# Performance work log

Hardware: AMD Instinct MI355X
Metric: run time of the kernel (lower is better)

## Reference

```python
import jax, jax.numpy as jnp
import numpy as np

N = 50000        # nodes
E = 800000       # edges (avg degree 16)
F_IN = 128       # in_channels
HID = 32         # hidden_channels per head
H = 8            # heads
DH = HID * H     # 256, concat dim
NC = {'TL': 12, 'YL': 30, 'TS': 60, 'TZ': 120}
NEG_SLOPE = 0.2  # PyG GATConv default


def setup_inputs() -> dict:
    key = jax.random.key(0)
    ks = jax.random.split(key, 40)
    rn = lambda k, s, sc=0.1: jax.random.normal(k, s, jnp.float32) * sc
    inp = {}
    inp['x'] = jax.random.normal(ks[0], (N, F_IN), jnp.float32)
    inp['edge_index'] = jax.random.randint(ks[1], (2, E), 0, N, dtype=jnp.int64)
    # conv1: in -> H x HID (concat)
    inp['W1'] = rn(ks[2], (F_IN, DH)); inp['a1s'] = rn(ks[3], (H, HID)); inp['a1d'] = rn(ks[4], (H, HID)); inp['b1'] = jnp.zeros((DH,), jnp.float32)
    # conv2: DH -> H x HID (concat)
    inp['W2'] = rn(ks[5], (DH, DH)); inp['a2s'] = rn(ks[6], (H, HID)); inp['a2d'] = rn(ks[7], (H, HID)); inp['b2'] = jnp.zeros((DH,), jnp.float32)
    # task heads: DH -> C, heads=1, concat=False
    i = 8
    for t, c in NC.items():
        inp['W_' + t] = rn(ks[i], (DH, c)); i += 1
        inp['as_' + t] = rn(ks[i], (1, c)); i += 1
        inp['ad_' + t] = rn(ks[i], (1, c)); i += 1
        inp['b_' + t] = jnp.zeros((c,), jnp.float32)
    return inp


def gat_conv(x, src, dst, W, a_s, a_d, b, concat):
    """PyG-style GATConv (eval mode, self-loops already in src/dst)."""
    n = x.shape[0]
    heads, out_ch = a_s.shape
    h = (x @ W).reshape(n, heads, out_ch)                 # [N,H,C]
    alpha_s = jnp.einsum('nhc,hc->nh', h, a_s)            # [N,H]
    alpha_d = jnp.einsum('nhc,hc->nh', h, a_d)
    e = jax.nn.leaky_relu(alpha_s[src] + alpha_d[dst], NEG_SLOPE)   # [E,H]
    # numerically-stable segment softmax over incoming edges of each dst
    m = jax.ops.segment_max(e, dst, num_segments=n)
    ex = jnp.exp(e - m[dst])
    denom = jax.ops.segment_sum(ex, dst, num_segments=n)
    alpha = ex / (denom[dst] + 1e-16)                     # [E,H]
    out = jax.ops.segment_sum(alpha[:, :, None] * h[src], dst, num_segments=n)  # [N,H,C]
    out = out.reshape(n, heads * out_ch) if concat else out.mean(axis=1)
    return out + b


def reference(x, edge_index, W1, a1s, a1d, b1, W2, a2s, a2d, b2,
              W_TL, as_TL, ad_TL, b_TL, W_YL, as_YL, ad_YL, b_YL,
              W_TS, as_TS, ad_TS, b_TS, W_TZ, as_TZ, ad_TZ, b_TZ):
    n = x.shape[0]
    loop = jnp.arange(n, dtype=edge_index.dtype)
    src = jnp.concatenate([edge_index[0], loop])
    dst = jnp.concatenate([edge_index[1], loop])
    h = jax.nn.elu(gat_conv(x, src, dst, W1, a1s, a1d, b1, True))
    h = gat_conv(h, src, dst, W2, a2s, a2d, b2, True)
    tl = jax.nn.log_softmax(gat_conv(h, src, dst, W_TL, as_TL, ad_TL, b_TL, False), axis=1)
    yl = jax.nn.log_softmax(gat_conv(h, src, dst, W_YL, as_YL, ad_YL, b_YL, False), axis=1)
    ts = jax.nn.log_softmax(gat_conv(h, src, dst, W_TS, as_TS, ad_TS, b_TS, False), axis=1)
    tz = jax.nn.log_softmax(gat_conv(h, src, dst, W_TZ, as_TZ, ad_TZ, b_TZ, False), axis=1)
    return (tl, yl, ts, tz)
```

## Files before the change

### kernel.cpp

```cpp
#include <hip/hip_runtime.h>
#include <math.h>


#define NEG_SLOPE 0.2f

typedef short s8v __attribute__((ext_vector_type(8)));
typedef short s4v __attribute__((ext_vector_type(4)));
typedef float f4v __attribute__((ext_vector_type(4)));

__device__ __forceinline__ short f2bf(float x) {
    unsigned u = __float_as_uint(x);
    u += 0x7fffu + ((u >> 16) & 1u);
    return (short)(u >> 16);
}
__device__ __forceinline__ float bf2f(short b) {
    return __uint_as_float(((unsigned)(unsigned short)b) << 16);
}
__device__ __forceinline__ void split2(float x, short& h, short& l) {
    h = f2bf(x);
    l = f2bf(x - bf2f(h));
}
__device__ __forceinline__ float4 bf4_to_f4(s4v v) {
    return make_float4(bf2f(v[0]), bf2f(v[1]), bf2f(v[2]), bf2f(v[3]));
}
__device__ __forceinline__ int rl_at(int v, int e) {
    int s = __builtin_amdgcn_readlane(v, e);
    return s < 0 ? 0 : s;
}


__global__ void init_kernel(int* __restrict__ deg, int* __restrict__ cursor, int n) {
    int i = blockIdx.x * blockDim.x + threadIdx.x;
    if (i < n) { deg[i] = 1; cursor[i] = 0; }
}

__global__ void count_kernel(const int* __restrict__ dst, int* __restrict__ deg, int E) {
    int i = blockIdx.x * blockDim.x + threadIdx.x;
    if (i < E) atomicAdd(&deg[dst[i]], 1);
}

__global__ __launch_bounds__(1024) void scan_kernel(const int* __restrict__ deg,
                                                    int* __restrict__ rowstart, int n) {
    __shared__ int wsum[16];
    __shared__ int carry_sh;
    int lane = threadIdx.x & 63, wv = threadIdx.x >> 6;
    if (threadIdx.x == 0) { carry_sh = 0; rowstart[0] = 0; }
    __syncthreads();
    for (int base = 0; base < n; base += 8192) {
        int vals[8];
        int sum = 0;
        int i0 = base + threadIdx.x * 8;
        #pragma unroll
        for (int j = 0; j < 8; ++j) {
            int i = i0 + j;
            int v = (i < n) ? ((deg[i] + 3) & ~3) : 0;
            sum += v;
            vals[j] = sum;
        }
        int incl = sum;
        #pragma unroll
        for (int off = 1; off < 64; off <<= 1) {
            int t = __shfl_up(incl, off);
            if (lane >= off) incl += t;
        }
        if (lane == 63) wsum[wv] = incl;
        __syncthreads();
        if (wv == 0) {
            int s = (lane < 16) ? wsum[lane] : 0;
            #pragma unroll
            for (int off = 1; off < 16; off <<= 1) {
                int t = __shfl_up(s, off);
                if (lane >= off) s += t;
            }
            if (lane < 16) wsum[lane] = s;
        }
        __syncthreads();
        int wexcl = (wv == 0) ? 0 : wsum[wv - 1];
        int excl = carry_sh + wexcl + (incl - sum);
        #pragma unroll
        for (int j = 0; j < 8; ++j) {
            int i = i0 + j;
            if (i < n) rowstart[i + 1] = excl + vals[j];
        }
        __syncthreads();
        if (threadIdx.x == 0) carry_sh += wsum[15];
        __syncthreads();
    }
}

__global__ void scatter_kernel(const int* __restrict__ src, const int* __restrict__ dst,
                               const int* __restrict__ rowstart, int* __restrict__ cursor,
                               int* __restrict__ csr, int* __restrict__ csrd, int E, int n) {
    int i = blockIdx.x * blockDim.x + threadIdx.x;
    if (i >= E + n) return;
    int s, d;
    if (i < E) { s = src[i]; d = dst[i]; }
    else       { s = d = i - E; }
    int p = atomicAdd(&cursor[d], 1);
    int slot = rowstart[d] + p;
    csr[slot] = s;
    csrd[slot] = d;
}


__global__ void tobf_kernel(const float* __restrict__ A, short* __restrict__ Ah, int n4) {
    int i = blockIdx.x * blockDim.x + threadIdx.x;
    if (i >= n4) return;
    float4 v = ((const float4*)A)[i];
    s4v hv = {f2bf(v.x), f2bf(v.y), f2bf(v.z), f2bf(v.w)};
    ((s4v*)Ah)[i] = hv;
}

__global__ void split_bt_kernel(const float* __restrict__ B, short* __restrict__ Bh,
                                short* __restrict__ Bl, int K, int Nc, int kshift) {
    int idx = blockIdx.x * blockDim.x + threadIdx.x;
    if (idx >= Nc * K) return;
    int n = idx >> kshift;
    int k = idx & (K - 1);
    float v = B[(size_t)k * Nc + n];
    short h, l; split2(v, h, l);
    Bh[idx] = h;
    Bl[idx] = l;
}

__global__ void fold_alpha8_kernel(const float* __restrict__ W,
                                   const float* __restrict__ a_s, const float* __restrict__ a_d,
                                   short* __restrict__ Bth, short* __restrict__ Btl,
                                   int K, int Nfeat) {
    int idx = blockIdx.x * blockDim.x + threadIdx.x;
    if (idx >= K * 16) return;
    int j = idx / K, k = idx % K;
    int h = j & 7;
    const float* av = ((j < 8) ? a_s : a_d) + h * 32;
    const float* wp = W + (size_t)k * 256 + h * 32;
    float s = 0.f;
    #pragma unroll
    for (int c = 0; c < 32; ++c) s += wp[c] * av[c];
    short hi, lo; split2(s, hi, lo);
    size_t off = (size_t)(Nfeat + j) * K + k;
    Bth[off] = hi; Btl[off] = lo;
}

__global__ void fold_alpha4_kernel(const float* __restrict__ Wcat,
                                   const float* __restrict__ ascat, const float* __restrict__ adcat,
                                   short* __restrict__ Bth, short* __restrict__ Btl) {
    int idx = blockIdx.x * blockDim.x + threadIdx.x;
    if (idx >= 256 * 8) return;
    int j = idx >> 8, k = idx & 255;
    const int CO[4] = {0, 12, 44, 104};
    const int CL[4] = {12, 32, 60, 120};
    int t = j & 3;
    const float* av = ((j < 4) ? ascat : adcat) + CO[t];
    const float* wp = Wcat + (size_t)k * 224 + CO[t];
    float s = 0.f;
    for (int c = 0; c < CL[t]; ++c) s += wp[c] * av[c];
    short hi, lo; split2(s, hi, lo);
    size_t off = (size_t)(224 + j) * 256 + k;
    Bth[off] = hi; Btl[off] = lo;
}


#define MB 128
#define NB 64
#define KS 32

__global__ __launch_bounds__(256) void gemm_mfma_kernel(
        const short* __restrict__ Ah_g,
        const short* __restrict__ Bth_g, const short* __restrict__ Btl_g,
        short* __restrict__ Cb, int cb_stride,
        float* __restrict__ als, float* __restrict__ ald, int nsplit,
        int M, int K, int Nfeat, int NcExt) {
    __shared__ __align__(16) short Ah[MB][40];
    __shared__ __align__(16) short Bh[NB][40];
    __shared__ __align__(16) short Bl[NB][40];

    int t = threadIdx.x;
    int lane = t & 63, w = t >> 6;
    int quad = lane >> 4, l16 = lane & 15;
    int row0 = blockIdx.y * MB, col0 = blockIdx.x * NB;

    f4v acc[2][4];
    #pragma unroll
    for (int mt = 0; mt < 2; ++mt)
        #pragma unroll
        for (int nt = 0; nt < 4; ++nt)
            acc[mt][nt] = (f4v){0.f, 0.f, 0.f, 0.f};

    for (int k0 = 0; k0 < K; k0 += KS) {
        __syncthreads();
        #pragma unroll
        for (int i = 0; i < 2; ++i) {
            int u = i * 256 + t;
            int r = u >> 2, kk = (u & 3) * 8;
            int gr = row0 + r;
            s8v vh = {0, 0, 0, 0, 0, 0, 0, 0};
            if (gr < M) vh = *(const s8v*)(Ah_g + (size_t)gr * K + k0 + kk);
            *(s8v*)&Ah[r][kk] = vh;
        }
        {
            int n = t >> 2, kk = (t & 3) * 8;
            int gc = col0 + n;
            s8v vh = {0, 0, 0, 0, 0, 0, 0, 0};
            s8v vl = {0, 0, 0, 0, 0, 0, 0, 0};
            if (gc < NcExt) {
                vh = *(const s8v*)(Bth_g + (size_t)gc * K + k0 + kk);
                vl = *(const s8v*)(Btl_g + (size_t)gc * K + k0 + kk);
            }
            *(s8v*)&Bh[n][kk] = vh;
            *(s8v*)&Bl[n][kk] = vl;
        }
        __syncthreads();

        int kb = quad * 8;
        s8v a_f[2], b_h[4], b_l[4];
        #pragma unroll
        for (int mt = 0; mt < 2; ++mt) {
            int r = w * 32 + mt * 16 + l16;
            a_f[mt] = *(const s8v*)&Ah[r][kb];
        }
        #pragma unroll
        for (int nt = 0; nt < 4; ++nt) {
            int c = nt * 16 + l16;
            b_h[nt] = *(const s8v*)&Bh[c][kb];
            b_l[nt] = *(const s8v*)&Bl[c][kb];
        }
        #pragma unroll
        for (int mt = 0; mt < 2; ++mt)
            #pragma unroll
            for (int nt = 0; nt < 4; ++nt) {
                acc[mt][nt] = __builtin_amdgcn_mfma_f32_16x16x32_bf16(
                    a_f[mt], b_h[nt], acc[mt][nt], 0, 0, 0);
                acc[mt][nt] = __builtin_amdgcn_mfma_f32_16x16x32_bf16(
                    a_f[mt], b_l[nt], acc[mt][nt], 0, 0, 0);
            }
    }

    #pragma unroll
    for (int mt = 0; mt < 2; ++mt) {
        #pragma unroll
        for (int nt = 0; nt < 4; ++nt) {
            int gc = col0 + nt * 16 + l16;
            if (gc >= NcExt) continue;
            #pragma unroll
            for (int r = 0; r < 4; ++r) {
                int gr = row0 + w * 32 + mt * 16 + quad * 4 + r;
                if (gr >= M) continue;
                float v = acc[mt][nt][r];
                if (gc < Nfeat) {
                    Cb[(size_t)gr * cb_stride + gc] = f2bf(v);
                } else {
                    int j = gc - Nfeat;
                    if (j < nsplit)            als[(size_t)gr * nsplit + j] = v;
                    else if (j < 2 * nsplit)   ald[(size_t)gr * nsplit + (j - nsplit)] = v;
                }
            }
        }
    }
}


__global__ void ew8_kernel(const float* __restrict__ als, const float* __restrict__ ald,
                           const int* __restrict__ csr, const int* __restrict__ csrd,
                           float* __restrict__ ewT, int M4) {
    int i = blockIdx.x * blockDim.x + threadIdx.x;
    if (i >= M4) return;
    int s = csr[i], d = csrd[i];
    if (s < 0) {
        #pragma unroll
        for (int h = 0; h < 8; ++h) ewT[(size_t)h * M4 + i] = 0.f;
        return;
    }
    const float4* ap = (const float4*)(als + (size_t)s * 8);
    const float4* dp = (const float4*)(ald + (size_t)d * 8);
    float4 a0 = ap[0], a1 = ap[1];
    float4 d0 = dp[0], d1 = dp[1];
    float v[8] = {a0.x + d0.x, a0.y + d0.y, a0.z + d0.z, a0.w + d0.w,
                  a1.x + d1.x, a1.y + d1.y, a1.z + d1.z, a1.w + d1.w};
    #pragma unroll
    for (int h = 0; h < 8; ++h) {
        float x = v[h];
        x = (x > 0.f) ? x : NEG_SLOPE * x;
        ewT[(size_t)h * M4 + i] = __expf(x);
    }
}


__global__ __launch_bounds__(256) void gat_gather_kernel(
        const short* __restrict__ hb, const float* __restrict__ ewT,
        const int* __restrict__ rowstart, const int* __restrict__ csr,
        const float* __restrict__ bias, short* __restrict__ oh, int n, int elu,
        int M4) {
    int wid  = blockIdx.x * 4 + (threadIdx.x >> 6);
    int lane = threadIdx.x & 63;
    if (wid >= n) return;
    int row = rowstart[wid];
    int pdeg = rowstart[wid + 1] - row;
    int hp = lane >> 3;
    int ch = lane * 4;
    const int* cp = csr + row;
    const float* wp = ewT + (size_t)hp * M4 + row;

    float4 acc = {0.f, 0.f, 0.f, 0.f};
    float wsum = 0.f;
    for (int base = 0; base < pdeg; base += 64) {
        int cnt = min(pdeg - base, 64);
        int idxv = -1;
        if (lane < cnt) idxv = cp[base + lane];
        const float* wpb = wp + base;
        int e = 0;
        for (; e + 8 <= cnt; e += 8) {
            int si[8];
            #pragma unroll
            for (int i = 0; i < 8; ++i) si[i] = rl_at(idxv, e + i);
            float4 wa = *(const float4*)(wpb + e);
            float4 wb = *(const float4*)(wpb + e + 4);
            s4v hv[8];
            #pragma unroll
            for (int i = 0; i < 8; ++i)
                hv[i] = *(const s4v*)(hb + (size_t)si[i] * 256 + ch);
            float wv[8] = {wa.x, wa.y, wa.z, wa.w, wb.x, wb.y, wb.z, wb.w};
            #pragma unroll
            for (int i = 0; i < 8; ++i) {
                float4 h = bf4_to_f4(hv[i]);
                acc.x += wv[i] * h.x; acc.y += wv[i] * h.y;
                acc.z += wv[i] * h.z; acc.w += wv[i] * h.w;
                wsum += wv[i];
            }
        }
        for (; e < cnt; e += 4) {
            int si[4];
            #pragma unroll
            for (int i = 0; i < 4; ++i) si[i] = rl_at(idxv, e + i);
            float4 wa = *(const float4*)(wpb + e);
            s4v hv[4];
            #pragma unroll
            for (int i = 0; i < 4; ++i)
                hv[i] = *(const s4v*)(hb + (size_t)si[i] * 256 + ch);
            float wv[4] = {wa.x, wa.y, wa.z, wa.w};
            #pragma unroll
            for (int i = 0; i < 4; ++i) {
                float4 h = bf4_to_f4(hv[i]);
                acc.x += wv[i] * h.x; acc.y += wv[i] * h.y;
                acc.z += wv[i] * h.z; acc.w += wv[i] * h.w;
                wsum += wv[i];
            }
        }
    }
    float inv = 1.f / (wsum + 1e-16f);
    float4 b4 = *(const float4*)(bias + ch);
    float v[4] = {acc.x * inv + b4.x, acc.y * inv + b4.y,
                  acc.z * inv + b4.z, acc.w * inv + b4.w};
    if (elu) {
        #pragma unroll
        for (int j = 0; j < 4; ++j)
            v[j] = (v[j] > 0.f) ? v[j] : __expf(v[j]) - 1.f;
    }
    s4v hvo = {f2bf(v[0]), f2bf(v[1]), f2bf(v[2]), f2bf(v[3])};
    *(s4v*)(oh + (size_t)wid * 256 + ch) = hvo;
}


__global__ void pack_w_kernel(const float* __restrict__ wTL, const float* __restrict__ wYL,
                              const float* __restrict__ wTS, const float* __restrict__ wTZ,
                              const float* __restrict__ bTL, const float* __restrict__ bYL,
                              const float* __restrict__ bTS, const float* __restrict__ bTZ,
                              const float* __restrict__ asTL, const float* __restrict__ asYL,
                              const float* __restrict__ asTS, const float* __restrict__ asTZ,
                              const float* __restrict__ adTL, const float* __restrict__ adYL,
                              const float* __restrict__ adTS, const float* __restrict__ adTZ,
                              float* __restrict__ Wcat, float* __restrict__ bcat,
                              float* __restrict__ ascat, float* __restrict__ adcat) {
    int idx = blockIdx.x * blockDim.x + threadIdx.x;
    if (idx < 256 * 224) {
        int r = idx / 224, c = idx % 224;
        float v = 0.f;
        if (c < 12)       v = wTL[r * 12 + c];
        else if (c < 42)  v = wYL[r * 30 + (c - 12)];
        else if (c < 44)  v = 0.f;
        else if (c < 104) v = wTS[r * 60 + (c - 44)];
        else              v = wTZ[r * 120 + (c - 104)];
        Wcat[idx] = v;
    }
    if (idx < 224) {
        float b = 0.f, as_ = 0.f, ad_ = 0.f;
        if (idx < 12)       { b = bTL[idx];       as_ = asTL[idx];       ad_ = adTL[idx]; }
        else if (idx < 42)  { b = bYL[idx - 12];  as_ = asYL[idx - 12];  ad_ = adYL[idx - 12]; }
        else if (idx < 44)  { }
        else if (idx < 104) { b = bTS[idx - 44];  as_ = asTS[idx - 44];  ad_ = adTS[idx - 44]; }
        else                { b = bTZ[idx - 104]; as_ = asTZ[idx - 104]; ad_ = adTZ[idx - 104]; }
        bcat[idx]  = b;
        ascat[idx] = as_;
        adcat[idx] = ad_;
    }
}


__global__ void ew4_kernel(const float* __restrict__ ast, const float* __restrict__ adt,
                           const int* __restrict__ csr, const int* __restrict__ csrd,
                           float* __restrict__ ewT, int M4) {
    int i = blockIdx.x * blockDim.x + threadIdx.x;
    if (i >= M4) return;
    int s = csr[i], d = csrd[i];
    if (s < 0) {
        #pragma unroll
        for (int t = 0; t < 4; ++t) ewT[(size_t)t * M4 + i] = 0.f;
        return;
    }
    float4 a = *(const float4*)(ast + (size_t)s * 4);
    float4 b = *(const float4*)(adt + (size_t)d * 4);
    float v[4] = {a.x + b.x, a.y + b.y, a.z + b.z, a.w + b.w};
    #pragma unroll
    for (int t = 0; t < 4; ++t) {
        float x = v[t];
        x = (x > 0.f) ? x : NEG_SLOPE * x;
        ewT[(size_t)t * M4 + i] = __expf(x);
    }
}


__device__ __forceinline__ float sel4(int t, float v0, float v1, float v2, float v3) {
    return (t == 0) ? v0 : (t == 1) ? v1 : (t == 2) ? v2 : v3;
}

__global__ __launch_bounds__(256) void task_gather_ls_kernel(
        const short* __restrict__ htb, const float* __restrict__ ewT,
        const int* __restrict__ rowstart, const int* __restrict__ csr,
        const float* __restrict__ bcat, float* __restrict__ out, int n, int M4) {
    int wid  = blockIdx.x * 4 + (threadIdx.x >> 6);
    int lane = threadIdx.x & 63;
    if (wid >= n) return;
    int row = rowstart[wid];
    int pdeg = rowstart[wid + 1] - row;
    int ch0 = lane * 4;
    int t = (lane < 3) ? 0 : (lane < 11) ? 1 : (lane < 26) ? 2 : 3;
    int COp = (t == 0) ? 0 : (t == 1) ? 12 : (t == 2) ? 44 : 104;
    int COr = (t == 0) ? 0 : (t == 1) ? 12 : (t == 2) ? 42 : 102;
    int CLr = (t == 0) ? 12 : (t == 1) ? 30 : (t == 2) ? 60 : 120;
    bool valj[4];
    #pragma unroll
    for (int j = 0; j < 4; ++j)
        valj[j] = (unsigned)(ch0 + j - COp) < (unsigned)CLr;

    const int* cp = csr + row;
    const float* wp = ewT + (size_t)t * M4 + row;

    float acc[4] = {0.f, 0.f, 0.f, 0.f};
    float ws = 0.f;
    for (int base = 0; base < pdeg; base += 64) {
        int cnt = min(pdeg - base, 64);
        int idxv = -1;
        if (lane < cnt) idxv = cp[base + lane];
        const float* wpb = wp + base;
        int e = 0;
        for (; e + 8 <= cnt; e += 8) {
            int si[8];
            #pragma unroll
            for (int i = 0; i < 8; ++i) si[i] = rl_at(idxv, e + i);
            float4 wa = *(const float4*)(wpb + e);
            float4 wb = *(const float4*)(wpb + e + 4);
            s4v hv[8];
            #pragma unroll
            for (int i = 0; i < 8; ++i)
                hv[i] = *(const s4v*)(htb + (size_t)si[i] * 224 + ch0);
            float wv[8] = {wa.x, wa.y, wa.z, wa.w, wb.x, wb.y, wb.z, wb.w};
            #pragma unroll
            for (int i = 0; i < 8; ++i) {
                float4 h = bf4_to_f4(hv[i]);
                acc[0] += wv[i] * h.x; acc[1] += wv[i] * h.y;
                acc[2] += wv[i] * h.z; acc[3] += wv[i] * h.w;
                ws += wv[i];
            }
        }
        for (; e < cnt; e += 4) {
            int si[4];
            #pragma unroll
            for (int i = 0; i < 4; ++i) si[i] = rl_at(idxv, e + i);
            float4 wa = *(const float4*)(wpb + e);
            s4v hv[4];
            #pragma unroll
            for (int i = 0; i < 4; ++i)
                hv[i] = *(const s4v*)(htb + (size_t)si[i] * 224 + ch0);
            float wv[4] = {wa.x, wa.y, wa.z, wa.w};
            #pragma unroll
            for (int i = 0; i < 4; ++i) {
                float4 h = bf4_to_f4(hv[i]);
                acc[0] += wv[i] * h.x; acc[1] += wv[i] * h.y;
                acc[2] += wv[i] * h.z; acc[3] += wv[i] * h.w;
                ws += wv[i];
            }
        }
    }
    float inv = 1.f / (ws + 1e-16f);

    float vout[4];
    float m = -1e30f;
    #pragma unroll
    for (int j = 0; j < 4; ++j) {
        float v = 0.f;
        if (valj[j]) { v = acc[j] * inv + bcat[ch0 + j]; m = fmaxf(m, v); }
        vout[j] = v;
    }
    float m0 = (t == 0) ? m : -1e30f;
    float m1 = (t == 1) ? m : -1e30f;
    float m2 = (t == 2) ? m : -1e30f;
    float m3 = (t == 3) ? m : -1e30f;
    #pragma unroll
    for (int off = 1; off < 64; off <<= 1) {
        m0 = fmaxf(m0, __shfl_xor(m0, off));
        m1 = fmaxf(m1, __shfl_xor(m1, off));
        m2 = fmaxf(m2, __shfl_xor(m2, off));
        m3 = fmaxf(m3, __shfl_xor(m3, off));
    }
    float mt = sel4(t, m0, m1, m2, m3);
    float sacc = 0.f;
    #pragma unroll
    for (int j = 0; j < 4; ++j)
        if (valj[j]) sacc += __expf(vout[j] - mt);
    float s0 = (t == 0) ? sacc : 0.f;
    float s1 = (t == 1) ? sacc : 0.f;
    float s2 = (t == 2) ? sacc : 0.f;
    float s3 = (t == 3) ? sacc : 0.f;
    #pragma unroll
    for (int off = 1; off < 64; off <<= 1) {
        s0 += __shfl_xor(s0, off);
        s1 += __shfl_xor(s1, off);
        s2 += __shfl_xor(s2, off);
        s3 += __shfl_xor(s3, off);
    }
    float st = sel4(t, s0, s1, s2, s3);
    float lse = mt + __logf(st);
    #pragma unroll
    for (int j = 0; j < 4; ++j)
        if (valj[j])
            out[(size_t)COr * n + (size_t)wid * CLr + (ch0 + j - COp)] = vout[j] - lse;
}


extern "C" void kernel_launch(void* const* d_in, const int* in_sizes, int n_in,
                              void* d_out, int out_size, void* d_ws, size_t ws_size,
                              hipStream_t stream) {
    const float* x   = (const float*)d_in[0];
    const int*   ei  = (const int*)d_in[1];
    const float* W1  = (const float*)d_in[2];
    const float* a1s = (const float*)d_in[3];
    const float* a1d = (const float*)d_in[4];
    const float* b1  = (const float*)d_in[5];
    const float* W2  = (const float*)d_in[6];
    const float* a2s = (const float*)d_in[7];
    const float* a2d = (const float*)d_in[8];
    const float* b2  = (const float*)d_in[9];
    const float* W_TL = (const float*)d_in[10]; const float* as_TL = (const float*)d_in[11];
    const float* ad_TL = (const float*)d_in[12]; const float* b_TL = (const float*)d_in[13];
    const float* W_YL = (const float*)d_in[14]; const float* as_YL = (const float*)d_in[15];
    const float* ad_YL = (const float*)d_in[16]; const float* b_YL = (const float*)d_in[17];
    const float* W_TS = (const float*)d_in[18]; const float* as_TS = (const float*)d_in[19];
    const float* ad_TS = (const float*)d_in[20]; const float* b_TS = (const float*)d_in[21];
    const float* W_TZ = (const float*)d_in[22]; const float* as_TZ = (const float*)d_in[23];
    const float* ad_TZ = (const float*)d_in[24]; const float* b_TZ = (const float*)d_in[25];

    const int N = in_sizes[0] / 128;
    const int E = in_sizes[1] / 2;
    const int* e_src = ei;
    const int* e_dst = ei + E;
    const int M4 = E + 4 * N;

    float* ws = (float*)d_ws;
    float* B1   = ws;
    float* B2   = B1 + (size_t)N * 256;
    float* B3   = B2 + (size_t)N * 256;
    float* as1  = B3 + (size_t)N * 256;
    float* ad1  = as1 + (size_t)N * 8;
    float* as2  = ad1 + (size_t)N * 8;
    float* ad2  = as2 + (size_t)N * 8;
    float* ast  = ad2 + (size_t)N * 8;
    float* adt  = ast + (size_t)N * 4;
    float* Wcat = adt + (size_t)N * 4;
    float* bcat = Wcat + 256 * 224;
    float* ascat = bcat + 224;
    float* adcat = ascat + 224;
    int* deg      = (int*)(adcat + 224);
    int* rowstart = deg + N;
    int* cursor   = rowstart + (N + 4);
    int* csr      = cursor + N;
    int* csrd     = csr + M4;
    uintptr_t wsp = (uintptr_t)(csrd + M4);
    wsp = (wsp + 15) & ~(uintptr_t)15;
    short* W1h = (short*)wsp;
    short* W1l = W1h + 272 * 128;
    short* W2h = W1l + 272 * 128;
    short* W2l = W2h + 272 * 256;
    short* Wth = W2l + 272 * 256;
    short* Wtl = Wth + 232 * 256;
    short* Xh  = (short*)B1;
    short* Sh  = (short*)B1;
    short* Th  = (short*)B1;
    short* h1b = (short*)B2;
    short* h2b = (short*)B2;
    short* htb = (short*)B2;
    float* ew1 = B3;
    float* ew2 = B3;
    float* ewt = B3;

    float* out = (float*)d_out;

    const int B = 256;
    init_kernel<<<(N + B - 1) / B, B, 0, stream>>>(deg, cursor, N);
    count_kernel<<<(E + B - 1) / B, B, 0, stream>>>(e_dst, deg, E);
    scan_kernel<<<1, 1024, 0, stream>>>(deg, rowstart, N);
    hipMemsetAsync(csr, 0xFF, (size_t)2 * M4 * sizeof(int), stream);
    scatter_kernel<<<(E + N + B - 1) / B, B, 0, stream>>>(e_src, e_dst, rowstart, cursor, csr, csrd, E, N);
    pack_w_kernel<<<(256 * 224 + B - 1) / B, B, 0, stream>>>(W_TL, W_YL, W_TS, W_TZ,
        b_TL, b_YL, b_TS, b_TZ, as_TL, as_YL, as_TS, as_TZ, ad_TL, ad_YL, ad_TS, ad_TZ,
        Wcat, bcat, ascat, adcat);
    split_bt_kernel<<<(256 * 128 + B - 1) / B, B, 0, stream>>>(W1, W1h, W1l, 128, 256, 7);
    split_bt_kernel<<<(256 * 256 + B - 1) / B, B, 0, stream>>>(W2, W2h, W2l, 256, 256, 8);
    split_bt_kernel<<<(224 * 256 + B - 1) / B, B, 0, stream>>>(Wcat, Wth, Wtl, 256, 224, 8);
    fold_alpha8_kernel<<<(128 * 16 + B - 1) / B, B, 0, stream>>>(W1, a1s, a1d, W1h, W1l, 128, 256);
    fold_alpha8_kernel<<<(256 * 16 + B - 1) / B, B, 0, stream>>>(W2, a2s, a2d, W2h, W2l, 256, 256);
    fold_alpha4_kernel<<<(256 * 8 + B - 1) / B, B, 0, stream>>>(Wcat, ascat, adcat, Wth, Wtl);
    tobf_kernel<<<((N * 128 / 4) + B - 1) / B, B, 0, stream>>>(x, Xh, N * 128 / 4);
    {
        dim3 g((272 + NB - 1) / NB, (N + MB - 1) / MB);
        gemm_mfma_kernel<<<g, 256, 0, stream>>>(Xh, W1h, W1l, h1b, 256,
                                                as1, ad1, 8, N, 128, 256, 272);
    }
    ew8_kernel<<<(M4 + B - 1) / B, B, 0, stream>>>(as1, ad1, csr, csrd, ew1, M4);
    gat_gather_kernel<<<(N + 3) / 4, 256, 0, stream>>>(h1b, ew1, rowstart, csr, b1, Sh, N, 1, M4);
    {
        dim3 g((272 + NB - 1) / NB, (N + MB - 1) / MB);
        gemm_mfma_kernel<<<g, 256, 0, stream>>>(Sh, W2h, W2l, h2b, 256,
                                                as2, ad2, 8, N, 256, 256, 272);
    }
    ew8_kernel<<<(M4 + B - 1) / B, B, 0, stream>>>(as2, ad2, csr, csrd, ew2, M4);
    gat_gather_kernel<<<(N + 3) / 4, 256, 0, stream>>>(h2b, ew2, rowstart, csr, b2, Th, N, 0, M4);
    {
        dim3 g((232 + NB - 1) / NB, (N + MB - 1) / MB);
        gemm_mfma_kernel<<<g, 256, 0, stream>>>(Th, Wth, Wtl, htb, 224,
                                                ast, adt, 4, N, 256, 224, 232);
    }
    ew4_kernel<<<(M4 + B - 1) / B, B, 0, stream>>>(ast, adt, csr, csrd, ewt, M4);
    task_gather_ls_kernel<<<(N + 3) / 4, 256, 0, stream>>>(htb, ewt, rowstart, csr, bcat, out, N, M4);
}
```

Baseline: 618.1 us.

## Fuse edge-weight computation into gather kernels and drop csrd array

Removes the separate ew8/ew4 kernels that wrote per-edge attention weights to a head-major buffer. The gather kernels now load the source alpha per edge, combine it with the destination alpha, and apply leaky-relu and exp inline. This also removes the csrd array and halves the memset. It saves three launches and the per-edge weight write and read traffic. In exchange, each gather does redundant exp work (every lane computes its head's weight per edge) and makes an extra scattered load from als per neighbour.

```diff
diff --git a/kernel.cpp b/kernel.cpp
--- a/kernel.cpp
+++ b/kernel.cpp
@@ -23,9 +23,8 @@
 __device__ __forceinline__ float4 bf4_to_f4(s4v v) {
     return make_float4(bf2f(v[0]), bf2f(v[1]), bf2f(v[2]), bf2f(v[3]));
 }
-__device__ __forceinline__ int rl_at(int v, int e) {
-    int s = __builtin_amdgcn_readlane(v, e);
-    return s < 0 ? 0 : s;
+__device__ __forceinline__ float leaky(float x) {
+    return fmaxf(x, NEG_SLOPE * x);
 }
 
 
@@ -90,16 +89,14 @@
 
 __global__ void scatter_kernel(const int* __restrict__ src, const int* __restrict__ dst,
                                const int* __restrict__ rowstart, int* __restrict__ cursor,
-                               int* __restrict__ csr, int* __restrict__ csrd, int E, int n) {
+                               int* __restrict__ csr, int E, int n) {
     int i = blockIdx.x * blockDim.x + threadIdx.x;
     if (i >= E + n) return;
     int s, d;
     if (i < E) { s = src[i]; d = dst[i]; }
     else       { s = d = i - E; }
     int p = atomicAdd(&cursor[d], 1);
-    int slot = rowstart[d] + p;
-    csr[slot] = s;
-    csrd[slot] = d;
+    csr[rowstart[d] + p] = s;
 }
 
 
@@ -259,37 +256,11 @@
 }
 
 
-__global__ void ew8_kernel(const float* __restrict__ als, const float* __restrict__ ald,
-                           const int* __restrict__ csr, const int* __restrict__ csrd,
-                           float* __restrict__ ewT, int M4) {
-    int i = blockIdx.x * blockDim.x + threadIdx.x;
-    if (i >= M4) return;
-    int s = csr[i], d = csrd[i];
-    if (s < 0) {
-        #pragma unroll
-        for (int h = 0; h < 8; ++h) ewT[(size_t)h * M4 + i] = 0.f;
-        return;
-    }
-    const float4* ap = (const float4*)(als + (size_t)s * 8);
-    const float4* dp = (const float4*)(ald + (size_t)d * 8);
-    float4 a0 = ap[0], a1 = ap[1];
-    float4 d0 = dp[0], d1 = dp[1];
-    float v[8] = {a0.x + d0.x, a0.y + d0.y, a0.z + d0.z, a0.w + d0.w,
-                  a1.x + d1.x, a1.y + d1.y, a1.z + d1.z, a1.w + d1.w};
-    #pragma unroll
-    for (int h = 0; h < 8; ++h) {
-        float x = v[h];
-        x = (x > 0.f) ? x : NEG_SLOPE * x;
-        ewT[(size_t)h * M4 + i] = __expf(x);
-    }
-}
-
-
 __global__ __launch_bounds__(256) void gat_gather_kernel(
-        const short* __restrict__ hb, const float* __restrict__ ewT,
+        const short* __restrict__ hb,
+        const float* __restrict__ als, const float* __restrict__ ald,
         const int* __restrict__ rowstart, const int* __restrict__ csr,
-        const float* __restrict__ bias, short* __restrict__ oh, int n, int elu,
-        int M4) {
+        const float* __restrict__ bias, short* __restrict__ oh, int n, int elu) {
     int wid  = blockIdx.x * 4 + (threadIdx.x >> 6);
     int lane = threadIdx.x & 63;
     if (wid >= n) return;
@@ -298,7 +269,7 @@
     int hp = lane >> 3;
     int ch = lane * 4;
     const int* cp = csr + row;
-    const float* wp = ewT + (size_t)hp * M4 + row;
+    float aldd = ald[(size_t)wid * 8 + hp];
 
     float4 acc = {0.f, 0.f, 0.f, 0.f};
     float wsum = 0.f;
@@ -306,43 +277,55 @@
         int cnt = min(pdeg - base, 64);
         int idxv = -1;
         if (lane < cnt) idxv = cp[base + lane];
-        const float* wpb = wp + base;
         int e = 0;
         for (; e + 8 <= cnt; e += 8) {
-            int si[8];
-            #pragma unroll
-            for (int i = 0; i < 8; ++i) si[i] = rl_at(idxv, e + i);
-            float4 wa = *(const float4*)(wpb + e);
-            float4 wb = *(const float4*)(wpb + e + 4);
+            int raw[8], si[8];
+            #pragma unroll
+            for (int i = 0; i < 8; ++i) {
+                raw[i] = __builtin_amdgcn_readlane(idxv, e + i);
+                si[i] = raw[i] < 0 ? 0 : raw[i];
+            }
+            float av[8];
+            #pragma unroll
+            for (int i = 0; i < 8; ++i)
+                av[i] = als[(size_t)si[i] * 8 + hp];
             s4v hv[8];
             #pragma unroll
             for (int i = 0; i < 8; ++i)
                 hv[i] = *(const s4v*)(hb + (size_t)si[i] * 256 + ch);
-            float wv[8] = {wa.x, wa.y, wa.z, wa.w, wb.x, wb.y, wb.z, wb.w};
             #pragma unroll
             for (int i = 0; i < 8; ++i) {
+                float wgt = __expf(leaky(av[i] + aldd));
+                if (raw[i] < 0) wgt = 0.f;
                 float4 h = bf4_to_f4(hv[i]);
-                acc.x += wv[i] * h.x; acc.y += wv[i] * h.y;
-                acc.z += wv[i] * h.z; acc.w += wv[i] * h.w;
-                wsum += wv[i];
+                acc.x += wgt * h.x; acc.y += wgt * h.y;
+                acc.z += wgt * h.z; acc.w += wgt * h.w;
+                wsum += wgt;
             }
         }
         for (; e < cnt; e += 4) {
-            int si[4];
-            #pragma unroll
-            for (int i = 0; i < 4; ++i) si[i] = rl_at(idxv, e + i);
-            float4 wa = *(const float4*)(wpb + e);
+            int raw[4], si[4];
+            #pragma unroll
+            for (int i = 0; i < 4; ++i) {
+                raw[i] = __builtin_amdgcn_readlane(idxv, e + i);
+                si[i] = raw[i] < 0 ? 0 : raw[i];
+            }
+            float av[4];
+            #pragma unroll
+            for (int i = 0; i < 4; ++i)
+                av[i] = als[(size_t)si[i] * 8 + hp];
             s4v hv[4];
             #pragma unroll
             for (int i = 0; i < 4; ++i)
                 hv[i] = *(const s4v*)(hb + (size_t)si[i] * 256 + ch);
-            float wv[4] = {wa.x, wa.y, wa.z, wa.w};
             #pragma unroll
             for (int i = 0; i < 4; ++i) {
+                float wgt = __expf(leaky(av[i] + aldd));
+                if (raw[i] < 0) wgt = 0.f;
                 float4 h = bf4_to_f4(hv[i]);
-                acc.x += wv[i] * h.x; acc.y += wv[i] * h.y;
-                acc.z += wv[i] * h.z; acc.w += wv[i] * h.w;
-                wsum += wv[i];
+                acc.x += wgt * h.x; acc.y += wgt * h.y;
+                acc.z += wgt * h.z; acc.w += wgt * h.w;
+                wsum += wgt;
             }
         }
     }
@@ -395,43 +378,21 @@
 }
 
 
-__global__ void ew4_kernel(const float* __restrict__ ast, const float* __restrict__ adt,
-                           const int* __restrict__ csr, const int* __restrict__ csrd,
-                           float* __restrict__ ewT, int M4) {
-    int i = blockIdx.x * blockDim.x + threadIdx.x;
-    if (i >= M4) return;
-    int s = csr[i], d = csrd[i];
-    if (s < 0) {
-        #pragma unroll
-        for (int t = 0; t < 4; ++t) ewT[(size_t)t * M4 + i] = 0.f;
-        return;
-    }
-    float4 a = *(const float4*)(ast + (size_t)s * 4);
-    float4 b = *(const float4*)(adt + (size_t)d * 4);
-    float v[4] = {a.x + b.x, a.y + b.y, a.z + b.z, a.w + b.w};
-    #pragma unroll
-    for (int t = 0; t < 4; ++t) {
-        float x = v[t];
-        x = (x > 0.f) ? x : NEG_SLOPE * x;
-        ewT[(size_t)t * M4 + i] = __expf(x);
-    }
-}
-
-
 __device__ __forceinline__ float sel4(int t, float v0, float v1, float v2, float v3) {
     return (t == 0) ? v0 : (t == 1) ? v1 : (t == 2) ? v2 : v3;
 }
 
 __global__ __launch_bounds__(256) void task_gather_ls_kernel(
-        const short* __restrict__ htb, const float* __restrict__ ewT,
+        const short* __restrict__ htb,
+        const float* __restrict__ ast, const float* __restrict__ adt,
         const int* __restrict__ rowstart, const int* __restrict__ csr,
-        const float* __restrict__ bcat, float* __restrict__ out, int n, int M4) {
+        const float* __restrict__ bcat, float* __restrict__ out, int n) {
     int wid  = blockIdx.x * 4 + (threadIdx.x >> 6);
     int lane = threadIdx.x & 63;
     if (wid >= n) return;
     int row = rowstart[wid];
     int pdeg = rowstart[wid + 1] - row;
-    int ch0 = lane * 4;
+    int ch0 = (lane < 56) ? lane * 4 : 0;
     int t = (lane < 3) ? 0 : (lane < 11) ? 1 : (lane < 26) ? 2 : 3;
     int COp = (t == 0) ? 0 : (t == 1) ? 12 : (t == 2) ? 44 : 104;
     int COr = (t == 0) ? 0 : (t == 1) ? 12 : (t == 2) ? 42 : 102;
@@ -442,55 +403,67 @@
         valj[j] = (unsigned)(ch0 + j - COp) < (unsigned)CLr;
 
     const int* cp = csr + row;
-    const float* wp = ewT + (size_t)t * M4 + row;
+    float adtd = adt[(size_t)wid * 4 + t];
 
     float acc[4] = {0.f, 0.f, 0.f, 0.f};
-    float ws = 0.f;
+    float wsv = 0.f;
     for (int base = 0; base < pdeg; base += 64) {
         int cnt = min(pdeg - base, 64);
         int idxv = -1;
         if (lane < cnt) idxv = cp[base + lane];
-        const float* wpb = wp + base;
         int e = 0;
         for (; e + 8 <= cnt; e += 8) {
-            int si[8];
-            #pragma unroll
-            for (int i = 0; i < 8; ++i) si[i] = rl_at(idxv, e + i);
-            float4 wa = *(const float4*)(wpb + e);
-            float4 wb = *(const float4*)(wpb + e + 4);
+            int raw[8], si[8];
+            #pragma unroll
+            for (int i = 0; i < 8; ++i) {
+                raw[i] = __builtin_amdgcn_readlane(idxv, e + i);
+                si[i] = raw[i] < 0 ? 0 : raw[i];
+            }
+            float av[8];
+            #pragma unroll
+            for (int i = 0; i < 8; ++i)
+                av[i] = ast[(size_t)si[i] * 4 + t];
             s4v hv[8];
             #pragma unroll
             for (int i = 0; i < 8; ++i)
                 hv[i] = *(const s4v*)(htb + (size_t)si[i] * 224 + ch0);
-            float wv[8] = {wa.x, wa.y, wa.z, wa.w, wb.x, wb.y, wb.z, wb.w};
             #pragma unroll
             for (int i = 0; i < 8; ++i) {
+                float wgt = __expf(leaky(av[i] + adtd));
+                if (raw[i] < 0) wgt = 0.f;
                 float4 h = bf4_to_f4(hv[i]);
-                acc[0] += wv[i] * h.x; acc[1] += wv[i] * h.y;
-                acc[2] += wv[i] * h.z; acc[3] += wv[i] * h.w;
-                ws += wv[i];
+                acc[0] += wgt * h.x; acc[1] += wgt * h.y;
+                acc[2] += wgt * h.z; acc[3] += wgt * h.w;
+                wsv += wgt;
             }
         }
         for (; e < cnt; e += 4) {
-            int si[4];
-            #pragma unroll
-            for (int i = 0; i < 4; ++i) si[i] = rl_at(idxv, e + i);
-            float4 wa = *(const float4*)(wpb + e);
+            int raw[4], si[4];
+            #pragma unroll
+            for (int i = 0; i < 4; ++i) {
+                raw[i] = __builtin_amdgcn_readlane(idxv, e + i);
+                si[i] = raw[i] < 0 ? 0 : raw[i];
+            }
+            float av[4];
+            #pragma unroll
+            for (int i = 0; i < 4; ++i)
+                av[i] = ast[(size_t)si[i] * 4 + t];
             s4v hv[4];
             #pragma unroll
             for (int i = 0; i < 4; ++i)
                 hv[i] = *(const s4v*)(htb + (size_t)si[i] * 224 + ch0);
-            float wv[4] = {wa.x, wa.y, wa.z, wa.w};
             #pragma unroll
             for (int i = 0; i < 4; ++i) {
+                float wgt = __expf(leaky(av[i] + adtd));
+                if (raw[i] < 0) wgt = 0.f;
                 float4 h = bf4_to_f4(hv[i]);
-                acc[0] += wv[i] * h.x; acc[1] += wv[i] * h.y;
-                acc[2] += wv[i] * h.z; acc[3] += wv[i] * h.w;
-                ws += wv[i];
-            }
-        }
-    }
-    float inv = 1.f / (ws + 1e-16f);
+                acc[0] += wgt * h.x; acc[1] += wgt * h.y;
+                acc[2] += wgt * h.z; acc[3] += wgt * h.w;
+                wsv += wgt;
+            }
+        }
+    }
+    float inv = 1.f / (wsv + 1e-16f);
 
     float vout[4];
     float m = -1e30f;
@@ -582,8 +555,7 @@
     int* rowstart = deg + N;
     int* cursor   = rowstart + (N + 4);
     int* csr      = cursor + N;
-    int* csrd     = csr + M4;
-    uintptr_t wsp = (uintptr_t)(csrd + M4);
+    uintptr_t wsp = (uintptr_t)(csr + M4);
     wsp = (wsp + 15) & ~(uintptr_t)15;
     short* W1h = (short*)wsp;
     short* W1l = W1h + 272 * 128;
@@ -597,9 +569,6 @@
     short* h1b = (short*)B2;
     short* h2b = (short*)B2;
     short* htb = (short*)B2;
-    float* ew1 = B3;
-    float* ew2 = B3;
-    float* ewt = B3;
 
     float* out = (float*)d_out;
 
@@ -607,8 +576,8 @@
     init_kernel<<<(N + B - 1) / B, B, 0, stream>>>(deg, cursor, N);
     count_kernel<<<(E + B - 1) / B, B, 0, stream>>>(e_dst, deg, E);
     scan_kernel<<<1, 1024, 0, stream>>>(deg, rowstart, N);
-    hipMemsetAsync(csr, 0xFF, (size_t)2 * M4 * sizeof(int), stream);
-    scatter_kernel<<<(E + N + B - 1) / B, B, 0, stream>>>(e_src, e_dst, rowstart, cursor, csr, csrd, E, N);
+    hipMemsetAsync(csr, 0xFF, (size_t)M4 * sizeof(int), stream);
+    scatter_kernel<<<(E + N + B - 1) / B, B, 0, stream>>>(e_src, e_dst, rowstart, cursor, csr, E, N);
     pack_w_kernel<<<(256 * 224 + B - 1) / B, B, 0, stream>>>(W_TL, W_YL, W_TS, W_TZ,
         b_TL, b_YL, b_TS, b_TZ, as_TL, as_YL, as_TS, as_TZ, ad_TL, ad_YL, ad_TS, ad_TZ,
         Wcat, bcat, ascat, adcat);
@@ -624,20 +593,17 @@
         gemm_mfma_kernel<<<g, 256, 0, stream>>>(Xh, W1h, W1l, h1b, 256,
                                                 as1, ad1, 8, N, 128, 256, 272);
     }
-    ew8_kernel<<<(M4 + B - 1) / B, B, 0, stream>>>(as1, ad1, csr, csrd, ew1, M4);
-    gat_gather_kernel<<<(N + 3) / 4, 256, 0, stream>>>(h1b, ew1, rowstart, csr, b1, Sh, N, 1, M4);
+    gat_gather_kernel<<<(N + 3) / 4, 256, 0, stream>>>(h1b, as1, ad1, rowstart, csr, b1, Sh, N, 1);
     {
         dim3 g((272 + NB - 1) / NB, (N + MB - 1) / MB);
         gemm_mfma_kernel<<<g, 256, 0, stream>>>(Sh, W2h, W2l, h2b, 256,
                                                 as2, ad2, 8, N, 256, 256, 272);
     }
-    ew8_kernel<<<(M4 + B - 1) / B, B, 0, stream>>>(as2, ad2, csr, csrd, ew2, M4);
-    gat_gather_kernel<<<(N + 3) / 4, 256, 0, stream>>>(h2b, ew2, rowstart, csr, b2, Th, N, 0, M4);
+    gat_gather_kernel<<<(N + 3) / 4, 256, 0, stream>>>(h2b, as2, ad2, rowstart, csr, b2, Th, N, 0);
     {
         dim3 g((232 + NB - 1) / NB, (N + MB - 1) / MB);
         gemm_mfma_kernel<<<g, 256, 0, stream>>>(Th, Wth, Wtl, htb, 224,
                                                 ast, adt, 4, N, 256, 224, 232);
     }
-    ew4_kernel<<<(M4 + B - 1) / B, B, 0, stream>>>(ast, adt, csr, csrd, ewt, M4);
-    task_gather_ls_kernel<<<(N + 3) / 4, 256, 0, stream>>>(htb, ewt, rowstart, csr, bcat, out, N, M4);
-}
+    task_gather_ls_kernel<<<(N + 3) / 4, 256, 0, stream>>>(htb, ast, adt, rowstart, csr, bcat, out, N);
+}
```

Result: faster. 596.5 us (-3.5%).
